# Kernel optimization log

Measured on AMD Instinct MI355X. Metric: run time of the kernel, lower is better.

## Reference

```python
import jax, jax.numpy as jnp
import numpy as np

K, B, N, V = 16, 512, 4096, 32  # concepts, test batch, train points, concept cardinality
EPS = 1e-13


def setup_inputs() -> dict:
    key = jax.random.key(0)
    k1, k2, k3 = jax.random.split(key, 3)
    c_p = jax.random.normal(k1, (K, B, V), dtype=jnp.float32)          # concept logits per test sample
    c_in = jax.random.randint(k2, (N, K), 0, V, dtype=jnp.int32)        # train concept labels
    delta_in = jax.random.randint(k3, (N,), 0, 2).astype(jnp.float32)   # censoring indicators
    bandwidth = jnp.ones((1,), dtype=jnp.float32)
    return {"c_in": c_in, "delta_in": delta_in, "c_p": c_p, "bandwidth": bandwidth}


def _forward(c_in, delta_in, c_p, bandwidth):
    # ---- SimpleGauss kernel weights ----
    p = jax.nn.softmax(c_p, axis=-1)                       # [K, B, V]
    sum_sq = jnp.sum(p * p, axis=-1)                       # [K, B]
    # scatter_reduce(-1 at label) then sum of squares == sum(p^2) - 2*p[label] + 1
    idx = jnp.broadcast_to(c_in.T[:, None, :], (K, B, N))  # [K, B, N]
    gathered = jnp.take_along_axis(p, idx, axis=-1)        # [K, B, N]
    metric = jnp.sum(sum_sq[:, :, None] - 2.0 * gathered + 1.0, axis=0)  # [B, N]
    bw = jnp.clip(bandwidth, 0.1, 10.0)                    # [1]
    w = jnp.exp(-metric / bw)                              # [B, N]
    s = jnp.sum(w, axis=1, keepdims=True)                  # sum over train points (dim=-2 of [B,N,1])
    bad = s < EPS
    W = jnp.where(bad, 0.0, w / jnp.where(bad, 1.0, s))    # [B, N]

    # ---- Beran estimator chain ----
    w_cumsum = jnp.cumsum(W, axis=1)
    shifted = w_cumsum - W
    bad_idx = jnp.isclose(shifted, 1.0) | jnp.isclose(w_cumsum, 1.0)
    shifted = jnp.where(bad_idx, 0.0, shifted)
    wc = jnp.where(bad_idx, 0.0, w_cumsum)
    xi = jnp.log(1.0 - shifted) - jnp.log(1.0 - wc)        # [B, N]
    hazards = jnp.cumsum(delta_in[None, :] * xi, axis=1)
    surv_func = jnp.exp(-hazards)                          # [B, N]
    first_step = 1.0 - surv_func[:, :1]
    surv_steps = jnp.concatenate([first_step, surv_func[:, :-1] - surv_func[:, 1:]], axis=-1)
    s2 = jnp.sum(surv_steps, axis=-1, keepdims=True)
    bad2 = s2 < EPS
    surv_steps = jnp.where(bad2, 0.0, surv_steps / jnp.where(bad2, 1.0, s2))
    return surv_func, surv_steps


def reference(c_in, delta_in, c_p, bandwidth):
    return _forward(c_in, delta_in, c_p, bandwidth)
```

## Files before the change

kernel.cpp:

```cpp
#include <hip/hip_runtime.h>
#include <math.h>

#define K_ 16
#define B_ 512
#define N_ 4096
#define V_ 32
#define TPB 512
#define CH (N_ / TPB)
#define NW (TPB / 64)
#define EPS_ 1e-13f

__global__ __launch_bounds__(TPB) void beran_kernel(
    const int* __restrict__ c_in, const float* __restrict__ delta_in,
    const float* __restrict__ c_p, const float* __restrict__ bandwidth,
    float* __restrict__ out) {
  __shared__ float p2[K_][V_];
  __shared__ float wbuf[N_];
  __shared__ float sumsq[K_];
  __shared__ float wscan[NW];
  __shared__ float s_base;

  const int b = blockIdx.x;
  const int t = threadIdx.x;
  const int lane = t & 63;
  const int wid = t >> 6;

  {
    const int k = t >> 5;
    const int v = t & 31;
    float x = c_p[((size_t)k * B_ + b) * V_ + v];
    float m = x;
#pragma unroll
    for (int d = 1; d < 32; d <<= 1) m = fmaxf(m, __shfl_xor(m, d, 64));
    float e = __expf(x - m);
    float sum = e;
#pragma unroll
    for (int d = 1; d < 32; d <<= 1) sum += __shfl_xor(sum, d, 64);
    float p = e * (1.0f / sum);
    p2[k][v] = 2.0f * p;
    float ss = p * p;
#pragma unroll
    for (int d = 1; d < 32; d <<= 1) ss += __shfl_xor(ss, d, 64);
    if (v == 0) sumsq[k] = ss;
  }
  __syncthreads();
  if (t == 0) {
    float bs = 0.f;
#pragma unroll
    for (int k = 0; k < K_; k++) bs += sumsq[k];
    s_base = bs + (float)K_;
  }
  __syncthreads();
  const float base = s_base;
  float bw = bandwidth[0];
  bw = fminf(fmaxf(bw, 0.1f), 10.0f);
  const float invbw = 1.0f / bw;

  const int start = t * CH;
  const int4* crow = (const int4*)c_in;
  float lv[CH];
  float tot = 0.f;
#pragma unroll
  for (int i = 0; i < CH; i++) {
    const int n = start + i;
    int4 a = crow[n * 4 + 0];
    int4 bb = crow[n * 4 + 1];
    int4 cc = crow[n * 4 + 2];
    int4 dd = crow[n * 4 + 3];
    float g = p2[0][a.x] + p2[1][a.y] + p2[2][a.z] + p2[3][a.w]
            + p2[4][bb.x] + p2[5][bb.y] + p2[6][bb.z] + p2[7][bb.w]
            + p2[8][cc.x] + p2[9][cc.y] + p2[10][cc.z] + p2[11][cc.w]
            + p2[12][dd.x] + p2[13][dd.y] + p2[14][dd.z] + p2[15][dd.w];
    float w = __expf(-(base - g) * invbw);
    lv[i] = w;
    tot += w;
  }
  float inc = tot;
#pragma unroll
  for (int d = 1; d < 64; d <<= 1) {
    float u = __shfl_up(inc, d, 64);
    if (lane >= d) inc += u;
  }
  if (lane == 63) wscan[wid] = inc;
  __syncthreads();
  float s = 0.f, woff = 0.f;
#pragma unroll
  for (int j = 0; j < NW; j++) {
    float v = wscan[j];
    s += v;
    if (j < wid) woff += v;
  }
  const float inv_s = (s < EPS_) ? 0.f : 1.0f / s;
  float rawp = woff + (inc - tot);

  const float4* dl4 = (const float4*)delta_in;
  float dl[CH];
#pragma unroll
  for (int j = 0; j < CH / 4; j++) {
    float4 d4 = dl4[t * (CH / 4) + j];
    dl[j * 4 + 0] = d4.x; dl[j * 4 + 1] = d4.y;
    dl[j * 4 + 2] = d4.z; dl[j * 4 + 3] = d4.w;
  }
  const float thr = 1.001e-5f;
#pragma unroll
  for (int i = 0; i < CH; i++) {
    float sh = rawp * inv_s;
    rawp += lv[i];
    float wc = rawp * inv_s;
    float y = 0.f;
    bool bad = (fabsf(sh - 1.f) <= thr) || (fabsf(wc - 1.f) <= thr);
    if (dl[i] != 0.f && !bad)
      y = dl[i] * (__logf(1.f - sh) - __logf(1.f - wc));
    lv[i] = y;
  }
  __syncthreads();

  float tot2 = 0.f;
#pragma unroll
  for (int i = 0; i < CH; i++) tot2 += lv[i];
  float inc2 = tot2;
#pragma unroll
  for (int d = 1; d < 64; d <<= 1) {
    float u = __shfl_up(inc2, d, 64);
    if (lane >= d) inc2 += u;
  }
  if (lane == 63) wscan[wid] = inc2;
  __syncthreads();
  float hoff = 0.f;
#pragma unroll
  for (int j = 0; j < NW; j++) if (j < wid) hoff += wscan[j];
  float h = hoff + (inc2 - tot2);
#pragma unroll
  for (int i = 0; i < CH; i++) {
    h += lv[i];
    wbuf[start + i] = __expf(-h);
  }
  __syncthreads();

  const float s2 = 1.0f - wbuf[N_ - 1];
  const float inv2 = (s2 < EPS_) ? 0.f : 1.0f / s2;
  float* out_s = out + (size_t)b * N_;
  float* out_t = out + (size_t)B_ * N_ + (size_t)b * N_;
  for (int n = t; n < N_; n += TPB) {
    float sv = wbuf[n];
    float pv = (n == 0) ? 1.0f : wbuf[n - 1];
    out_s[n] = sv;
    out_t[n] = (pv - sv) * inv2;
  }
}

extern "C" void kernel_launch(void* const* d_in, const int* in_sizes, int n_in,
                              void* d_out, int out_size, void* d_ws, size_t ws_size,
                              hipStream_t stream) {
  const int* c_in = (const int*)d_in[0];
  const float* delta_in = (const float*)d_in[1];
  const float* c_p = (const float*)d_in[2];
  const float* bandwidth = (const float*)d_in[3];
  float* outp = (float*)d_out;
  hipLaunchKernelGGL(beran_kernel, dim3(B_), dim3(TPB), 0, stream,
                     c_in, delta_in, c_p, bandwidth, outp);
}
```

Measured before the change: 83.87 us.

## Coalesce c_in loads via strided indexing and stage weights through padded LDS

The weight computation now has each thread handle points strided by the block size, so the int4 loads of c_in are coalesced across the wavefront instead of each thread reading a contiguous chunk. The weights are written to LDS with a padding swizzle, then read back in contiguous per-thread chunks for the scan; the padding is meant to avoid bank conflicts. It also removes one barrier by letting every thread compute the base, moves the delta loads earlier so they overlap the scan, uses a separate scan buffer, and derives s2 from the total hazard rather than reading LDS after a barrier. The LDS round trip adds a barrier and some LDS traffic in exchange.

```diff
diff --git a/kernel.cpp b/kernel.cpp
--- a/kernel.cpp
+++ b/kernel.cpp
@@ -9,16 +9,18 @@
 #define CH (N_ / TPB)
 #define NW (TPB / 64)
 #define EPS_ 1e-13f
+#define SWZ(n) ((n) + ((n) >> 5))
+#define WBUF_SZ (N_ + (N_ >> 5))
 
 __global__ __launch_bounds__(TPB) void beran_kernel(
     const int* __restrict__ c_in, const float* __restrict__ delta_in,
     const float* __restrict__ c_p, const float* __restrict__ bandwidth,
     float* __restrict__ out) {
   __shared__ float p2[K_][V_];
-  __shared__ float wbuf[N_];
   __shared__ float sumsq[K_];
+  __shared__ float wbuf[WBUF_SZ];
   __shared__ float wscan[NW];
-  __shared__ float s_base;
+  __shared__ float wscan2[NW];
 
   const int b = blockIdx.x;
   const int t = threadIdx.x;
@@ -44,25 +46,17 @@
     if (v == 0) sumsq[k] = ss;
   }
   __syncthreads();
-  if (t == 0) {
-    float bs = 0.f;
+
+  float base = (float)K_;
 #pragma unroll
-    for (int k = 0; k < K_; k++) bs += sumsq[k];
-    s_base = bs + (float)K_;
-  }
-  __syncthreads();
-  const float base = s_base;
-  float bw = bandwidth[0];
-  bw = fminf(fmaxf(bw, 0.1f), 10.0f);
+  for (int k = 0; k < K_; k++) base += sumsq[k];
+  float bw = fminf(fmaxf(bandwidth[0], 0.1f), 10.0f);
   const float invbw = 1.0f / bw;
 
-  const int start = t * CH;
   const int4* crow = (const int4*)c_in;
-  float lv[CH];
-  float tot = 0.f;
 #pragma unroll
-  for (int i = 0; i < CH; i++) {
-    const int n = start + i;
+  for (int j = 0; j < CH; j++) {
+    const int n = t + j * TPB;
     int4 a = crow[n * 4 + 0];
     int4 bb = crow[n * 4 + 1];
     int4 cc = crow[n * 4 + 2];
@@ -71,10 +65,15 @@
             + p2[4][bb.x] + p2[5][bb.y] + p2[6][bb.z] + p2[7][bb.w]
             + p2[8][cc.x] + p2[9][cc.y] + p2[10][cc.z] + p2[11][cc.w]
             + p2[12][dd.x] + p2[13][dd.y] + p2[14][dd.z] + p2[15][dd.w];
-    float w = __expf(-(base - g) * invbw);
-    lv[i] = w;
-    tot += w;
+    wbuf[SWZ(n)] = __expf(-(base - g) * invbw);
   }
+  __syncthreads();
+
+  const int start = t * CH;
+  float lv[CH];
+  float tot = 0.f;
+#pragma unroll
+  for (int i = 0; i < CH; i++) { lv[i] = wbuf[SWZ(start + i)]; tot += lv[i]; }
   float inc = tot;
 #pragma unroll
   for (int d = 1; d < 64; d <<= 1) {
@@ -82,6 +81,15 @@
     if (lane >= d) inc += u;
   }
   if (lane == 63) wscan[wid] = inc;
+
+  const float4* dl4 = (const float4*)delta_in;
+  float dl[CH];
+#pragma unroll
+  for (int j = 0; j < CH / 4; j++) {
+    float4 d4 = dl4[t * (CH / 4) + j];
+    dl[j * 4 + 0] = d4.x; dl[j * 4 + 1] = d4.y;
+    dl[j * 4 + 2] = d4.z; dl[j * 4 + 3] = d4.w;
+  }
   __syncthreads();
   float s = 0.f, woff = 0.f;
 #pragma unroll
@@ -93,14 +101,6 @@
   const float inv_s = (s < EPS_) ? 0.f : 1.0f / s;
   float rawp = woff + (inc - tot);
 
-  const float4* dl4 = (const float4*)delta_in;
-  float dl[CH];
-#pragma unroll
-  for (int j = 0; j < CH / 4; j++) {
-    float4 d4 = dl4[t * (CH / 4) + j];
-    dl[j * 4 + 0] = d4.x; dl[j * 4 + 1] = d4.y;
-    dl[j * 4 + 2] = d4.z; dl[j * 4 + 3] = d4.w;
-  }
   const float thr = 1.001e-5f;
 #pragma unroll
   for (int i = 0; i < CH; i++) {
@@ -113,7 +113,6 @@
       y = dl[i] * (__logf(1.f - sh) - __logf(1.f - wc));
     lv[i] = y;
   }
-  __syncthreads();
 
   float tot2 = 0.f;
 #pragma unroll
@@ -124,26 +123,32 @@
     float u = __shfl_up(inc2, d, 64);
     if (lane >= d) inc2 += u;
   }
-  if (lane == 63) wscan[wid] = inc2;
+  if (lane == 63) wscan2[wid] = inc2;
   __syncthreads();
-  float hoff = 0.f;
+  float hoff = 0.f, htot = 0.f;
 #pragma unroll
-  for (int j = 0; j < NW; j++) if (j < wid) hoff += wscan[j];
+  for (int j = 0; j < NW; j++) {
+    float v = wscan2[j];
+    htot += v;
+    if (j < wid) hoff += v;
+  }
   float h = hoff + (inc2 - tot2);
 #pragma unroll
   for (int i = 0; i < CH; i++) {
     h += lv[i];
-    wbuf[start + i] = __expf(-h);
+    wbuf[SWZ(start + i)] = __expf(-h);
   }
+  const float s2 = 1.0f - __expf(-htot);
+  const float inv2 = (s2 < EPS_) ? 0.f : 1.0f / s2;
   __syncthreads();
 
-  const float s2 = 1.0f - wbuf[N_ - 1];
-  const float inv2 = (s2 < EPS_) ? 0.f : 1.0f / s2;
   float* out_s = out + (size_t)b * N_;
   float* out_t = out + (size_t)B_ * N_ + (size_t)b * N_;
-  for (int n = t; n < N_; n += TPB) {
-    float sv = wbuf[n];
-    float pv = (n == 0) ? 1.0f : wbuf[n - 1];
+#pragma unroll
+  for (int j = 0; j < CH; j++) {
+    const int n = t + j * TPB;
+    float sv = wbuf[SWZ(n)];
+    float pv = (n == 0) ? 1.0f : wbuf[SWZ(n - 1)];
     out_s[n] = sv;
     out_t[n] = (pv - sv) * inv2;
   }
```

After: 76.91 us. 1.09x faster.
